# Kernel tuning notes

Hardware: AMD Instinct MI355X
Metric: run time of the kernel (lower is better)

Reference implementation:

```python
import jax, jax.numpy as jnp
import numpy as np

B, P, X, Y, F = 32768, 128, 30, 30, 6
T = 0.001  # softmax temperature from the module


def setup_inputs() -> dict:
    key = jax.random.key(0)
    k1, k2, k3, k4 = jax.random.split(key, 4)
    feats = jax.random.normal(k1, (B, 2, F), dtype=jnp.float32)
    # coordinate columns (ss_x, ss_y, es_x, es_y): integer grid coords stored as floats
    coords = jax.random.randint(k2, (B, 2, 4), 0, X).astype(jnp.float32)
    phi = jnp.concatenate([feats, coords], axis=-1)  # [B, 2, F+4]
    succ_feats = jax.random.normal(k3, (P, X, Y, F), dtype=jnp.float32)
    w = jax.random.normal(k4, (F,), dtype=jnp.float32)  # linear1.weight (1,F) squeezed
    return {"phi": phi, "succ_feats": succ_feats, "w": w}


def _get_vals(succ_feats, w, xs, ys):
    # xs, ys: [B, 2] float coords (exact ints); succ_feats: [P, X, Y, F]
    p, x_dim, y_dim, f = succ_feats.shape
    idx = xs.astype(jnp.int32) * y_dim + ys.astype(jnp.int32)        # [B, 2]
    sf = succ_feats.reshape(p, x_dim * y_dim, f)
    g = sf[:, idx]                                                   # [P, B, 2, F] gather
    vs = jnp.einsum('pbtf,f->bpt', g, w)                             # [B, P, 2]
    wts = jax.nn.softmax(vs / T, axis=1)                             # softmax over policies
    return jnp.sum(wts * vs, axis=1)                                 # [B, 2]


def reference(phi, succ_feats, w):
    f = w.shape[0]
    pr = jnp.einsum('btf,f->bt', phi[:, :, :f], w)                   # [B, 2]
    v_ss = _get_vals(succ_feats, w, phi[:, :, f], phi[:, :, f + 1])  # start states
    v_es = _get_vals(succ_feats, w, phi[:, :, f + 2], phi[:, :, f + 3])  # end states
    # rw = v_stw = v_s0w = 1 (preference_weights=None)
    delta_er = pr + (v_es - v_ss)                                    # [B, 2]
    left = delta_er[:, 0:1]
    right = delta_er[:, 1:2]
    left_pred = jax.nn.sigmoid(left - right)                         # [B, 1]
    right_pred = jax.nn.sigmoid(right - left)                        # [B, 1]
    return jnp.stack([left_pred, right_pred], axis=1)                # [B, 2, 1]
```

## Files before the change

### kernel.cpp

```cpp
#include <hip/hip_runtime.h>
#include <math.h>

#define B_N   32768
#define P_N   128
#define X_N   30
#define Y_N   30
#define F_N   6
#define CELLS (X_N * Y_N)
#define INV_T 1000.0f

__global__ __launch_bounds__(64) void build_table_kernel(
    const float* __restrict__ sf, const float* __restrict__ w,
    float* __restrict__ V)
{
    const int cell = blockIdx.x;
    const int lane = threadIdx.x;

    float wv[F_N];
#pragma unroll
    for (int f = 0; f < F_N; ++f) wv[f] = w[f];

    const float* b0 = sf + (size_t)lane        * (CELLS * F_N) + (size_t)cell * F_N;
    const float* b1 = sf + (size_t)(lane + 64) * (CELLS * F_N) + (size_t)cell * F_N;

    float d0 = 0.f, d1 = 0.f;
#pragma unroll
    for (int f = 0; f < F_N; ++f) {
        d0 = fmaf(b0[f], wv[f], d0);
        d1 = fmaf(b1[f], wv[f], d1);
    }

    float m = fmaxf(d0, d1);
#pragma unroll
    for (int off = 32; off >= 1; off >>= 1)
        m = fmaxf(m, __shfl_xor(m, off, 64));

    float e0 = __expf((d0 - m) * INV_T);
    float e1 = __expf((d1 - m) * INV_T);
    float num = e0 * d0 + e1 * d1;
    float den = e0 + e1;
#pragma unroll
    for (int off = 32; off >= 1; off >>= 1) {
        num += __shfl_xor(num, off, 64);
        den += __shfl_xor(den, off, 64);
    }

    if (lane == 0) V[cell] = num / den;
}

__global__ __launch_bounds__(256) void finalize_kernel(
    const float* __restrict__ phi, const float* __restrict__ w,
    const float* __restrict__ V, float* __restrict__ out)
{
    __shared__ float Vs[CELLS];
    for (int i = threadIdx.x; i < CELLS; i += blockDim.x)
        Vs[i] = V[i];
    __syncthreads();

    const int b = blockIdx.x * blockDim.x + threadIdx.x;
    if (b >= B_N) return;

    const float w0 = w[0], w1 = w[1], w2 = w[2], w3 = w[3], w4 = w[4], w5 = w[5];

    const float4* p4 = (const float4*)(phi + (size_t)b * 20);
    float4 c0 = p4[0];
    float4 c1 = p4[1];
    float4 c2 = p4[2];
    float4 c3 = p4[3];
    float4 c4 = p4[4];

    float pr0 = c0.x*w0 + c0.y*w1 + c0.z*w2 + c0.w*w3 + c1.x*w4 + c1.y*w5;
    float pr1 = c2.z*w0 + c2.w*w1 + c3.x*w2 + c3.y*w3 + c3.z*w4 + c3.w*w5;

    int iss0 = (int)c1.z * Y_N + (int)c1.w;
    int ies0 = (int)c2.x * Y_N + (int)c2.y;
    int iss1 = (int)c4.x * Y_N + (int)c4.y;
    int ies1 = (int)c4.z * Y_N + (int)c4.w;

    float d0 = pr0 + Vs[ies0] - Vs[iss0];
    float d1 = pr1 + Vs[ies1] - Vs[iss1];

    float x = d0 - d1;
    float s0 = 1.0f / (1.0f + expf(-x));
    float s1 = 1.0f / (1.0f + expf(x));

    float2* o2 = (float2*)(out + (size_t)b * 2);
    *o2 = make_float2(s0, s1);
}

extern "C" void kernel_launch(void* const* d_in, const int* in_sizes, int n_in,
                              void* d_out, int out_size, void* d_ws, size_t ws_size,
                              hipStream_t stream) {
    const float* phi = (const float*)d_in[0];
    const float* sf  = (const float*)d_in[1];
    const float* w   = (const float*)d_in[2];
    float* out = (float*)d_out;
    float* V   = (float*)d_ws;

    build_table_kernel<<<CELLS, 64, 0, stream>>>(sf, w, V);
    finalize_kernel<<<(B_N + 255) / 256, 256, 0, stream>>>(phi, w, V, out);
}
```

Measured before the change: 65.52 us.

## Fuse table build and finalize into one cooperative kernel with grid sync

Merges the per-cell softmax table build and the per-batch finalize into a single cooperative kernel separated by a grid-wide barrier. Each block builds four cells with one wave each, using float2 loads, then each thread computes one output side. This aims to remove the second launch and the inter-kernel gap. In exchange it adds grid sync cost, and phi is read redundantly by both threads of a pair.

```diff
diff --git a/kernel.cpp b/kernel.cpp
--- a/kernel.cpp
+++ b/kernel.cpp
@@ -1,5 +1,8 @@
 #include <hip/hip_runtime.h>
+#include <hip/hip_cooperative_groups.h>
 #include <math.h>
+
+namespace cg = cooperative_groups;
 
 #define B_N   32768
 #define P_N   128
@@ -7,60 +10,65 @@
 #define Y_N   30
 #define F_N   6
 #define CELLS (X_N * Y_N)
+#define ROW_F (CELLS * F_N)
 #define INV_T 1000.0f
 
-__global__ __launch_bounds__(64) void build_table_kernel(
-    const float* __restrict__ sf, const float* __restrict__ w,
-    float* __restrict__ V)
+__global__ __launch_bounds__(256) void fused_kernel(
+    const float* __restrict__ phi, const float* __restrict__ sf,
+    const float* __restrict__ w, float* __restrict__ V,
+    float* __restrict__ out)
 {
-    const int cell = blockIdx.x;
-    const int lane = threadIdx.x;
+    cg::grid_group grid = cg::this_grid();
 
-    float wv[F_N];
+    const int tid  = threadIdx.x;
+    const int lane = tid & 63;
+    const int wave = tid >> 6;
+    const int cell = blockIdx.x * 4 + wave;
+
+    const float w0 = w[0], w1 = w[1], w2 = w[2],
+                w3 = w[3], w4 = w[4], w5 = w[5];
+
+    if (cell < CELLS) {
+        const float* r0 = sf + (size_t)lane * ROW_F + cell * F_N;
+        const float* r1 = r0 + (size_t)64 * ROW_F;
+
+        float2 a0 = *(const float2*)(r0);
+        float2 a1 = *(const float2*)(r0 + 2);
+        float2 a2 = *(const float2*)(r0 + 4);
+        float2 b0 = *(const float2*)(r1);
+        float2 b1 = *(const float2*)(r1 + 2);
+        float2 b2 = *(const float2*)(r1 + 4);
+
+        float d0 = a0.x*w0 + a0.y*w1 + a1.x*w2 + a1.y*w3 + a2.x*w4 + a2.y*w5;
+        float d1 = b0.x*w0 + b0.y*w1 + b1.x*w2 + b1.y*w3 + b2.x*w4 + b2.y*w5;
+
+        float m = fmaxf(d0, d1);
 #pragma unroll
-    for (int f = 0; f < F_N; ++f) wv[f] = w[f];
+        for (int off = 32; off >= 1; off >>= 1)
+            m = fmaxf(m, __shfl_xor(m, off, 64));
 
-    const float* b0 = sf + (size_t)lane        * (CELLS * F_N) + (size_t)cell * F_N;
-    const float* b1 = sf + (size_t)(lane + 64) * (CELLS * F_N) + (size_t)cell * F_N;
+        float e0 = __expf((d0 - m) * INV_T);
+        float e1 = __expf((d1 - m) * INV_T);
+        float num = e0 * d0 + e1 * d1;
+        float den = e0 + e1;
+#pragma unroll
+        for (int off = 32; off >= 1; off >>= 1) {
+            num += __shfl_xor(num, off, 64);
+            den += __shfl_xor(den, off, 64);
+        }
 
-    float d0 = 0.f, d1 = 0.f;
-#pragma unroll
-    for (int f = 0; f < F_N; ++f) {
-        d0 = fmaf(b0[f], wv[f], d0);
-        d1 = fmaf(b1[f], wv[f], d1);
+        if (lane == 0) V[cell] = num / den;
     }
 
-    float m = fmaxf(d0, d1);
-#pragma unroll
-    for (int off = 32; off >= 1; off >>= 1)
-        m = fmaxf(m, __shfl_xor(m, off, 64));
+    grid.sync();
 
-    float e0 = __expf((d0 - m) * INV_T);
-    float e1 = __expf((d1 - m) * INV_T);
-    float num = e0 * d0 + e1 * d1;
-    float den = e0 + e1;
-#pragma unroll
-    for (int off = 32; off >= 1; off >>= 1) {
-        num += __shfl_xor(num, off, 64);
-        den += __shfl_xor(den, off, 64);
-    }
-
-    if (lane == 0) V[cell] = num / den;
-}
-
-__global__ __launch_bounds__(256) void finalize_kernel(
-    const float* __restrict__ phi, const float* __restrict__ w,
-    const float* __restrict__ V, float* __restrict__ out)
-{
     __shared__ float Vs[CELLS];
-    for (int i = threadIdx.x; i < CELLS; i += blockDim.x)
-        Vs[i] = V[i];
+    for (int i = tid; i < CELLS; i += 256) Vs[i] = V[i];
     __syncthreads();
 
-    const int b = blockIdx.x * blockDim.x + threadIdx.x;
-    if (b >= B_N) return;
-
-    const float w0 = w[0], w1 = w[1], w2 = w[2], w3 = w[3], w4 = w[4], w5 = w[5];
+    const int o    = blockIdx.x * 256 + tid;
+    const int b    = o >> 1;
+    const int side = o & 1;
 
     const float4* p4 = (const float4*)(phi + (size_t)b * 20);
     float4 c0 = p4[0];
@@ -80,12 +88,8 @@
     float d0 = pr0 + Vs[ies0] - Vs[iss0];
     float d1 = pr1 + Vs[ies1] - Vs[iss1];
 
-    float x = d0 - d1;
-    float s0 = 1.0f / (1.0f + expf(-x));
-    float s1 = 1.0f / (1.0f + expf(x));
-
-    float2* o2 = (float2*)(out + (size_t)b * 2);
-    *o2 = make_float2(s0, s1);
+    float x = side ? (d1 - d0) : (d0 - d1);
+    out[o] = 1.0f / (1.0f + expf(-x));
 }
 
 extern "C" void kernel_launch(void* const* d_in, const int* in_sizes, int n_in,
@@ -97,6 +101,7 @@
     float* out = (float*)d_out;
     float* V   = (float*)d_ws;
 
-    build_table_kernel<<<CELLS, 64, 0, stream>>>(sf, w, V);
-    finalize_kernel<<<(B_N + 255) / 256, 256, 0, stream>>>(phi, w, V, out);
+    void* args[] = { (void*)&phi, (void*)&sf, (void*)&w, (void*)&V, (void*)&out };
+    hipLaunchCooperativeKernel(reinterpret_cast<void*>(fused_kernel),
+                               dim3(256), dim3(256), args, 0, stream);
 }
```

After: 100.1 us. +52.8%, slower.
